# Kernel tuning notes

Hardware: AMD Instinct MI355X
Metric: run time of the kernel (lower is better)

## Reference

```python
import jax, jax.numpy as jnp
import numpy as np

N_NODES = 100000
N_EDGES = 1600000
NODE_DIM = 64
HIDDEN = 64
T = 11


def _init_linear(key, d_in, d_out, bias=True):
    kw, kb = jax.random.split(key)
    lim = 1.0 / np.sqrt(d_in)
    W = jax.random.uniform(kw, (d_in, d_out), jnp.float32, -lim, lim)
    if bias:
        b = jax.random.uniform(kb, (d_out,), jnp.float32, -lim, lim)
        return W, b
    return W


def setup_inputs() -> dict:
    key = jax.random.key(0)
    ks = jax.random.split(key, 10)
    x = jax.random.normal(ks[0], (N_NODES, NODE_DIM), jnp.float32)
    edge_index = jax.random.randint(ks[1], (2, N_EDGES), 0, N_NODES, jnp.int64)
    time_span = jnp.arange(T, dtype=jnp.float32)
    # SAGEConv params: W_neigh (lin_l, with bias) applied to mean-aggregated
    # neighbors, W_root (lin_r, no bias) applied to the node itself.
    W1n, b1 = _init_linear(ks[2], NODE_DIM, HIDDEN)
    W1r = _init_linear(ks[3], NODE_DIM, HIDDEN, bias=False)
    W2n, b2 = _init_linear(ks[4], HIDDEN, HIDDEN)
    W2r = _init_linear(ks[5], HIDDEN, HIDDEN, bias=False)
    W3n, b3 = _init_linear(ks[6], HIDDEN, NODE_DIM)
    W3r = _init_linear(ks[7], HIDDEN, NODE_DIM, bias=False)
    Wd, bd = _init_linear(ks[8], NODE_DIM, 2)
    return {
        "x": x, "edge_index": edge_index, "time_span": time_span,
        "W1n": W1n, "b1": b1, "W1r": W1r,
        "W2n": W2n, "b2": b2, "W2r": W2r,
        "W3n": W3n, "b3": b3, "W3r": W3r,
        "Wd": Wd, "bd": bd,
    }


def _sage_conv(x, src, dst, deg_inv, Wn, bn, Wr):
    # gather source features, mean-aggregate onto targets (PyG SAGEConv 'mean')
    agg = jax.ops.segment_sum(x[src], dst, num_segments=N_NODES)  # [N, d]
    mean = agg * deg_inv  # zero for isolated nodes
    return mean @ Wn + bn + x @ Wr


def reference(x, edge_index, time_span, W1n, b1, W1r, W2n, b2, W2r,
              W3n, b3, W3r, Wd, bd):
    src, dst = edge_index[0], edge_index[1]
    deg = jax.ops.segment_sum(jnp.ones((N_EDGES,), jnp.float32), dst,
                              num_segments=N_NODES)
    deg_inv = jnp.where(deg > 0, 1.0 / jnp.maximum(deg, 1.0), 0.0)[:, None]

    def ode_func(h):
        h1 = jax.nn.relu(_sage_conv(h, src, dst, deg_inv, W1n, b1, W1r))
        h2 = jax.nn.relu(_sage_conv(h1, src, dst, deg_inv, W2n, b2, W2r))
        return _sage_conv(h2, src, dst, deg_inv, W3n, b3, W3r)

    dts = time_span[1:] - time_span[:-1]  # euler fixed-step per interval

    def step(h, dt):
        h_new = h + dt * ode_func(h)
        return h_new, h_new

    _, xs = jax.lax.scan(step, x, dts)
    solution = jnp.concatenate([x[None], xs], axis=0)  # [T, N, node_dim]
    trajectories = solution @ Wd + bd  # [T, N, 2]
    return trajectories, solution
```

## Files before the change

### kernel.cpp

```cpp
#include <hip/hip_runtime.h>

#define NN 100000
#define NE 1600000
#define DIM 64
#define TT 11
#define NB_SCAN 391
#define NCH 13
#define CST 16

typedef unsigned short u16;
typedef unsigned int u32;

__device__ __forceinline__ u32 pack_bf16(float a, float b) {
    u32 ua = __float_as_uint(a);
    ua += 0x7fff + ((ua >> 16) & 1);
    u32 ub = __float_as_uint(b);
    ub += 0x7fff + ((ub >> 16) & 1);
    return (ua >> 16) | (ub & 0xffff0000u);
}
__device__ __forceinline__ float bf2f(u16 v) {
    return __uint_as_float(((u32)v) << 16);
}

__global__ void k_degc(const int* __restrict__ src, const int* __restrict__ dst,
                       int* __restrict__ deg, int* __restrict__ degc) {
    int e = blockIdx.x * blockDim.x + threadIdx.x;
    if (e < NE) {
        int d = dst[e], c = src[e] >> 13;
        atomicAdd(&deg[d], 1);
        atomicAdd(&degc[d * CST + c], 1);
    }
}

__global__ __launch_bounds__(256) void k_bsum(const int* __restrict__ deg,
                                              int* __restrict__ bsum) {
    __shared__ int s[256];
    int t = threadIdx.x;
    int i = blockIdx.x * 256 + t;
    s[t] = (i < NN) ? deg[i] : 0;
    __syncthreads();
    for (int off = 128; off >= 1; off >>= 1) {
        if (t < off) s[t] += s[t + off];
        __syncthreads();
    }
    if (t == 0) bsum[blockIdx.x] = s[0];
}

__global__ __launch_bounds__(512) void k_scan1(const int* __restrict__ bsum,
                                               int* __restrict__ bpre) {
    __shared__ int s[512];
    int t = threadIdx.x;
    int v0 = (t < NB_SCAN) ? bsum[t] : 0;
    s[t] = v0;
    __syncthreads();
    for (int off = 1; off < 512; off <<= 1) {
        int v = (t >= off) ? s[t - off] : 0;
        __syncthreads();
        s[t] += v;
        __syncthreads();
    }
    if (t < NB_SCAN) bpre[t] = s[t] - v0;
}

__global__ __launch_bounds__(256) void k_rowptr(const int* __restrict__ deg,
        const int* __restrict__ degc, const int* __restrict__ bpre,
        int* __restrict__ row_ptr, int* __restrict__ cursor16,
        float* __restrict__ deg_inv) {
    __shared__ int s[256];
    int t = threadIdx.x;
    int i = blockIdx.x * 256 + t;
    int d = (i < NN) ? deg[i] : 0;
    s[t] = d;
    __syncthreads();
    for (int off = 1; off < 256; off <<= 1) {
        int v = (t >= off) ? s[t - off] : 0;
        __syncthreads();
        s[t] += v;
        __syncthreads();
    }
    if (i < NN) {
        int excl = bpre[blockIdx.x] + s[t] - d;
        row_ptr[i] = excl;
        deg_inv[i] = d > 0 ? 1.0f / (float)d : 0.0f;
        int run = excl;
#pragma unroll
        for (int c = 0; c < NCH; ++c) {
            cursor16[i * CST + c] = run;
            run += degc[i * CST + c];
        }
        if (i == NN - 1) row_ptr[NN] = excl + d;
    }
}

__global__ void k_fillc(const int* __restrict__ src, const int* __restrict__ dst,
        int* __restrict__ cursor16, int* __restrict__ csr_src) {
    int e = blockIdx.x * blockDim.x + threadIdx.x;
    if (e < NE) {
        int sv = src[e];
        int p = atomicAdd(&cursor16[dst[e] * CST + (sv >> 13)], 1);
        csr_src[p] = sv;
    }
}

__global__ __launch_bounds__(256) void k_gather(const u16* __restrict__ hb,
        const int* __restrict__ row_ptr, const int* __restrict__ csr_src,
        const float* __restrict__ deg_inv, u16* __restrict__ Mb) {
    int wid = (int)((blockIdx.x * blockDim.x + threadIdx.x) >> 6);
    int lane = threadIdx.x & 63;
    if (wid >= NN) return;
    int sub = lane >> 3;
    int d4 = lane & 7;
    int b = row_ptr[wid], e = row_ptr[wid + 1];
    float di = deg_inv[wid];
    float a0[8] = {0, 0, 0, 0, 0, 0, 0, 0};
    float a1[8] = {0, 0, 0, 0, 0, 0, 0, 0};
    int i = b;
    for (; i + 16 <= e; i += 16) {
        int n0 = csr_src[i + sub];
        int n1 = csr_src[i + 8 + sub];
        uint4 v0 = *(const uint4*)(hb + ((size_t)n0 << 6) + d4 * 8);
        uint4 v1 = *(const uint4*)(hb + ((size_t)n1 << 6) + d4 * 8);
        const u32* w0 = (const u32*)&v0;
        const u32* w1 = (const u32*)&v1;
#pragma unroll
        for (int w = 0; w < 4; ++w) {
            a0[2 * w]     += __uint_as_float(w0[w] << 16);
            a0[2 * w + 1] += __uint_as_float(w0[w] & 0xffff0000u);
            a1[2 * w]     += __uint_as_float(w1[w] << 16);
            a1[2 * w + 1] += __uint_as_float(w1[w] & 0xffff0000u);
        }
    }
    if (i + 8 <= e) {
        int n0 = csr_src[i + sub];
        uint4 v0 = *(const uint4*)(hb + ((size_t)n0 << 6) + d4 * 8);
        const u32* w0 = (const u32*)&v0;
#pragma unroll
        for (int w = 0; w < 4; ++w) {
            a0[2 * w]     += __uint_as_float(w0[w] << 16);
            a0[2 * w + 1] += __uint_as_float(w0[w] & 0xffff0000u);
        }
        i += 8;
    }
    if (sub < e - i) {
        int n1 = csr_src[i + sub];
        uint4 v1 = *(const uint4*)(hb + ((size_t)n1 << 6) + d4 * 8);
        const u32* w1 = (const u32*)&v1;
#pragma unroll
        for (int w = 0; w < 4; ++w) {
            a1[2 * w]     += __uint_as_float(w1[w] << 16);
            a1[2 * w + 1] += __uint_as_float(w1[w] & 0xffff0000u);
        }
    }
    float s[8];
#pragma unroll
    for (int k = 0; k < 8; ++k) {
        float v = a0[k] + a1[k];
        v += __shfl_xor(v, 32);
        v += __shfl_xor(v, 16);
        v += __shfl_xor(v, 8);
        s[k] = v * di;
    }
    if (lane < 8) {
        uint4 p;
        p.x = pack_bf16(s[0], s[1]);
        p.y = pack_bf16(s[2], s[3]);
        p.z = pack_bf16(s[4], s[5]);
        p.w = pack_bf16(s[6], s[7]);
        *(uint4*)(Mb + ((size_t)wid << 6) + d4 * 8) = p;
    }
}

template <int MODE>
__global__ __launch_bounds__(256) void k_transform(
        const u16* __restrict__ Mb, const u16* __restrict__ Hb,
        const float* __restrict__ Wn, const float* __restrict__ bias,
        const float* __restrict__ Wr, const float* __restrict__ prev,
        const float* __restrict__ ts, int tstep, float* __restrict__ out,
        u16* __restrict__ out_b,
        const float* __restrict__ Wd, const float* __restrict__ bd,
        float* __restrict__ traj) {
    __shared__ float Ws[128 * 64];
    __shared__ float tp0[MODE ? 128 * 9 : 1];
    __shared__ float tp1[MODE ? 128 * 9 : 1];
    int tid = threadIdx.x;
    {
        const float4* wn4 = (const float4*)Wn;
        const float4* wr4 = (const float4*)Wr;
        float4* ws4 = (float4*)Ws;
        for (int i = tid; i < 2048; i += 256)
            ws4[i] = (i < 1024) ? wn4[i] : wr4[i - 1024];
    }
    __syncthreads();
    int jg = tid & 7, ng = tid >> 3;
    int nbase = blockIdx.x * 128 + ng * 4;
    int j0 = jg * 8;
    float acc[4][8];
#pragma unroll
    for (int i = 0; i < 4; ++i)
#pragma unroll
        for (int j = 0; j < 8; ++j) acc[i][j] = bias[j0 + j];
    int nidx[4];
    bool valid[4];
#pragma unroll
    for (int i = 0; i < 4; ++i) {
        int n = nbase + i;
        valid[i] = n < NN;
        nidx[i] = valid[i] ? n : 0;
    }
#pragma unroll 1
    for (int ph = 0; ph < 2; ++ph) {
        const u16* A = ph ? Hb : Mb;
        int wofs = ph ? 64 * 64 : 0;
        for (int k0 = 0; k0 < 64; k0 += 4) {
            float a[4][4];
#pragma unroll
            for (int i = 0; i < 4; ++i) {
                ushort4 r = *(const ushort4*)(A + ((size_t)nidx[i] << 6) + k0);
                a[i][0] = bf2f(r.x); a[i][1] = bf2f(r.y);
                a[i][2] = bf2f(r.z); a[i][3] = bf2f(r.w);
            }
#pragma unroll
            for (int kk = 0; kk < 4; ++kk) {
                float w[8];
                *(float4*)&w[0] = *(float4*)&Ws[wofs + (k0 + kk) * 64 + j0];
                *(float4*)&w[4] = *(float4*)&Ws[wofs + (k0 + kk) * 64 + j0 + 4];
#pragma unroll
                for (int i = 0; i < 4; ++i)
#pragma unroll
                    for (int j = 0; j < 8; ++j)
                        acc[i][j] = fmaf(a[i][kk], w[j], acc[i][j]);
            }
        }
    }
    float dt = 0.f, wd0[8], wd1[8];
    if (MODE == 1) {
        dt = ts[tstep + 1] - ts[tstep];
#pragma unroll
        for (int j = 0; j < 8; ++j) {
            wd0[j] = Wd[(j0 + j) * 2 + 0];
            wd1[j] = Wd[(j0 + j) * 2 + 1];
        }
    }
#pragma unroll
    for (int i = 0; i < 4; ++i) {
        float o[8];
        float p0 = 0.f, p1 = 0.f;
#pragma unroll
        for (int j = 0; j < 8; ++j) {
            float v = acc[i][j];
            if (MODE == 0) v = fmaxf(v, 0.f);
            else v = prev[(size_t)nidx[i] * 64 + j0 + j] + dt * v;
            o[j] = v;
            if (MODE == 1) { p0 = fmaf(v, wd0[j], p0); p1 = fmaf(v, wd1[j], p1); }
        }
        if (MODE == 1) {
            tp0[(ng * 4 + i) * 9 + jg] = p0;
            tp1[(ng * 4 + i) * 9 + jg] = p1;
        }
        if (valid[i]) {
            if (MODE == 1) {
                *(float4*)(out + (size_t)nidx[i] * 64 + j0) = *(float4*)&o[0];
                *(float4*)(out + (size_t)nidx[i] * 64 + j0 + 4) = *(float4*)&o[4];
            }
            uint4 pb;
            pb.x = pack_bf16(o[0], o[1]);
            pb.y = pack_bf16(o[2], o[3]);
            pb.z = pack_bf16(o[4], o[5]);
            pb.w = pack_bf16(o[6], o[7]);
            *(uint4*)(out_b + (size_t)nidx[i] * 64 + j0) = pb;
        }
    }
    if (MODE == 1) {
        __syncthreads();
        int node = tid >> 1, comp = tid & 1;
        const float* tp = comp ? tp1 : tp0;
        float s = bd[comp];
#pragma unroll
        for (int g = 0; g < 8; ++g) s += tp[node * 9 + g];
        int gnode = blockIdx.x * 128 + node;
        if (gnode < NN)
            traj[((size_t)(tstep + 1) * NN + gnode) * 2 + comp] = s;
    }
}

__global__ __launch_bounds__(256) void k_init(const float* __restrict__ x,
        const float* __restrict__ Wd, const float* __restrict__ bd,
        float* __restrict__ sol0, u16* __restrict__ xb,
        float* __restrict__ traj) {
    int n = blockIdx.x * blockDim.x + threadIdx.x;
    if (n >= NN) return;
    const float4* xr = (const float4*)(x + ((size_t)n << 6));
    float4* sr = (float4*)(sol0 + ((size_t)n << 6));
    uint4* br = (uint4*)(xb + ((size_t)n << 6));
    float p0 = bd[0], p1 = bd[1];
#pragma unroll
    for (int k8 = 0; k8 < 8; ++k8) {
        float4 v0 = xr[k8 * 2];
        float4 v1 = xr[k8 * 2 + 1];
        sr[k8 * 2] = v0;
        sr[k8 * 2 + 1] = v1;
        uint4 pb;
        pb.x = pack_bf16(v0.x, v0.y);
        pb.y = pack_bf16(v0.z, v0.w);
        pb.z = pack_bf16(v1.x, v1.y);
        pb.w = pack_bf16(v1.z, v1.w);
        br[k8] = pb;
        int k = k8 * 8;
        p0 = fmaf(v0.x, Wd[(k + 0) * 2], p0); p1 = fmaf(v0.x, Wd[(k + 0) * 2 + 1], p1);
        p0 = fmaf(v0.y, Wd[(k + 1) * 2], p0); p1 = fmaf(v0.y, Wd[(k + 1) * 2 + 1], p1);
        p0 = fmaf(v0.z, Wd[(k + 2) * 2], p0); p1 = fmaf(v0.z, Wd[(k + 2) * 2 + 1], p1);
        p0 = fmaf(v0.w, Wd[(k + 3) * 2], p0); p1 = fmaf(v0.w, Wd[(k + 3) * 2 + 1], p1);
        p0 = fmaf(v1.x, Wd[(k + 4) * 2], p0); p1 = fmaf(v1.x, Wd[(k + 4) * 2 + 1], p1);
        p0 = fmaf(v1.y, Wd[(k + 5) * 2], p0); p1 = fmaf(v1.y, Wd[(k + 5) * 2 + 1], p1);
        p0 = fmaf(v1.z, Wd[(k + 6) * 2], p0); p1 = fmaf(v1.z, Wd[(k + 6) * 2 + 1], p1);
        p0 = fmaf(v1.w, Wd[(k + 7) * 2], p0); p1 = fmaf(v1.w, Wd[(k + 7) * 2 + 1], p1);
    }
    traj[(size_t)n * 2 + 0] = p0;
    traj[(size_t)n * 2 + 1] = p1;
}

extern "C" void kernel_launch(void* const* d_in, const int* in_sizes, int n_in,
                              void* d_out, int out_size, void* d_ws, size_t ws_size,
                              hipStream_t stream) {
    const float* x = (const float*)d_in[0];
    const int* ei = (const int*)d_in[1];
    const float* ts = (const float*)d_in[2];
    const float* W1n = (const float*)d_in[3];
    const float* b1 = (const float*)d_in[4];
    const float* W1r = (const float*)d_in[5];
    const float* W2n = (const float*)d_in[6];
    const float* b2 = (const float*)d_in[7];
    const float* W2r = (const float*)d_in[8];
    const float* W3n = (const float*)d_in[9];
    const float* b3 = (const float*)d_in[10];
    const float* W3r = (const float*)d_in[11];
    const float* Wd = (const float*)d_in[12];
    const float* bd = (const float*)d_in[13];
    const int* src = ei;
    const int* dst = ei + NE;

    char* w = (char*)d_ws;
    int* deg = (int*)w;          w += (size_t)NN * 4;
    int* degc = (int*)w;         w += (size_t)NN * CST * 4;
    int* row_ptr = (int*)w;      w += (size_t)(NN + 1) * 4;
    int* cursor16 = (int*)w;     w += (size_t)NN * CST * 4;
    float* deg_inv = (float*)w;  w += (size_t)NN * 4;
    int* bsum = (int*)w;         w += (size_t)512 * 4;
    int* bpre = (int*)w;         w += (size_t)512 * 4;
    int* csr = (int*)w;          w += (size_t)NE * 4;
    u16* Mb = (u16*)w;           w += (size_t)NN * DIM * 2;
    u16* hb0 = (u16*)w;          w += (size_t)NN * DIM * 2;
    u16* hb1 = (u16*)w;          w += (size_t)NN * DIM * 2;
    u16* hb2 = (u16*)w;          w += (size_t)NN * DIM * 2;

    float* traj = (float*)d_out;
    float* sol = traj + (size_t)TT * NN * 2;

    hipMemsetAsync(deg, 0, (size_t)NN * (CST + 1) * 4, stream);
    k_degc<<<(NE + 255) / 256, 256, 0, stream>>>(src, dst, deg, degc);
    k_bsum<<<NB_SCAN, 256, 0, stream>>>(deg, bsum);
    k_scan1<<<1, 512, 0, stream>>>(bsum, bpre);
    k_rowptr<<<NB_SCAN, 256, 0, stream>>>(deg, degc, bpre, row_ptr, cursor16, deg_inv);
    k_fillc<<<(NE + 255) / 256, 256, 0, stream>>>(src, dst, cursor16, csr);
    k_init<<<NB_SCAN, 256, 0, stream>>>(x, Wd, bd, sol, hb0, traj);

    const int GB = (NN * 64 + 255) / 256;
    const int TB = (NN + 127) / 128;
    for (int t = 0; t < TT - 1; ++t) {
        float* st = sol + (size_t)t * NN * DIM;
        float* sn = st + (size_t)NN * DIM;
        k_gather<<<GB, 256, 0, stream>>>(hb0, row_ptr, csr, deg_inv, Mb);
        k_transform<0><<<TB, 256, 0, stream>>>(Mb, hb0, W1n, b1, W1r, nullptr,
                ts, t, nullptr, hb1, Wd, bd, traj);
        k_gather<<<GB, 256, 0, stream>>>(hb1, row_ptr, csr, deg_inv, Mb);
        k_transform<0><<<TB, 256, 0, stream>>>(Mb, hb1, W2n, b2, W2r, nullptr,
                ts, t, nullptr, hb2, Wd, bd, traj);
        k_gather<<<GB, 256, 0, stream>>>(hb2, row_ptr, csr, deg_inv, Mb);
        k_transform<1><<<TB, 256, 0, stream>>>(Mb, hb2, W3n, b3, W3r, st,
                ts, t, sn, hb0, Wd, bd, traj);
    }
}
```

Before: 2.725 ms.

## Gather 8 rows per wave with per-chunk neighbor counts for locality-ordered access

The gather kernel now assigns one 8-lane group per destination row, so a wave serves 8 rows instead of 1. Each group walks the row's neighbors chunk by chunk using stored per-source-chunk counts (u16 ccnt). Adjacent groups therefore touch source rows in the same 8192-node chunk at roughly the same time, which is meant to improve cache reuse and remove the cross-lane shuffle reduction. The separate degree array is dropped and degree is derived from degc. In exchange, lanes within a wave diverge when rows have different degrees or chunk counts, and each lane now issues one load at a time.

Measured after the change: 3.078 ms. 1.13x slower.

```diff
diff --git a/kernel.cpp b/kernel.cpp
--- a/kernel.cpp
+++ b/kernel.cpp
@@ -23,21 +23,22 @@
 }
 
 __global__ void k_degc(const int* __restrict__ src, const int* __restrict__ dst,
-                       int* __restrict__ deg, int* __restrict__ degc) {
+                       int* __restrict__ degc) {
     int e = blockIdx.x * blockDim.x + threadIdx.x;
-    if (e < NE) {
-        int d = dst[e], c = src[e] >> 13;
-        atomicAdd(&deg[d], 1);
-        atomicAdd(&degc[d * CST + c], 1);
-    }
-}
-
-__global__ __launch_bounds__(256) void k_bsum(const int* __restrict__ deg,
+    if (e < NE) atomicAdd(&degc[dst[e] * CST + (src[e] >> 13)], 1);
+}
+
+__global__ __launch_bounds__(256) void k_bsum(const int* __restrict__ degc,
                                               int* __restrict__ bsum) {
     __shared__ int s[256];
     int t = threadIdx.x;
     int i = blockIdx.x * 256 + t;
-    s[t] = (i < NN) ? deg[i] : 0;
+    int d = 0;
+    if (i < NN) {
+#pragma unroll
+        for (int c = 0; c < NCH; ++c) d += degc[i * CST + c];
+    }
+    s[t] = d;
     __syncthreads();
     for (int off = 128; off >= 1; off >>= 1) {
         if (t < off) s[t] += s[t + off];
@@ -62,14 +63,19 @@
     if (t < NB_SCAN) bpre[t] = s[t] - v0;
 }
 
-__global__ __launch_bounds__(256) void k_rowptr(const int* __restrict__ deg,
-        const int* __restrict__ degc, const int* __restrict__ bpre,
-        int* __restrict__ row_ptr, int* __restrict__ cursor16,
+__global__ __launch_bounds__(256) void k_rowptr(const int* __restrict__ degc,
+        const int* __restrict__ bpre, int* __restrict__ row_ptr,
+        int* __restrict__ cursor16, u16* __restrict__ ccnt,
         float* __restrict__ deg_inv) {
     __shared__ int s[256];
     int t = threadIdx.x;
     int i = blockIdx.x * 256 + t;
-    int d = (i < NN) ? deg[i] : 0;
+    int dc[NCH];
+    int d = 0;
+    if (i < NN) {
+#pragma unroll
+        for (int c = 0; c < NCH; ++c) { dc[c] = degc[i * CST + c]; d += dc[c]; }
+    }
     s[t] = d;
     __syncthreads();
     for (int off = 1; off < 256; off <<= 1) {
@@ -86,8 +92,11 @@
 #pragma unroll
         for (int c = 0; c < NCH; ++c) {
             cursor16[i * CST + c] = run;
-            run += degc[i * CST + c];
-        }
+            ccnt[i * CST + c] = (u16)dc[c];
+            run += dc[c];
+        }
+#pragma unroll
+        for (int c = NCH; c < CST; ++c) ccnt[i * CST + c] = 0;
         if (i == NN - 1) row_ptr[NN] = excl + d;
     }
 }
@@ -103,71 +112,43 @@
 }
 
 __global__ __launch_bounds__(256) void k_gather(const u16* __restrict__ hb,
-        const int* __restrict__ row_ptr, const int* __restrict__ csr_src,
-        const float* __restrict__ deg_inv, u16* __restrict__ Mb) {
-    int wid = (int)((blockIdx.x * blockDim.x + threadIdx.x) >> 6);
-    int lane = threadIdx.x & 63;
-    if (wid >= NN) return;
-    int sub = lane >> 3;
-    int d4 = lane & 7;
-    int b = row_ptr[wid], e = row_ptr[wid + 1];
-    float di = deg_inv[wid];
-    float a0[8] = {0, 0, 0, 0, 0, 0, 0, 0};
-    float a1[8] = {0, 0, 0, 0, 0, 0, 0, 0};
-    int i = b;
-    for (; i + 16 <= e; i += 16) {
-        int n0 = csr_src[i + sub];
-        int n1 = csr_src[i + 8 + sub];
-        uint4 v0 = *(const uint4*)(hb + ((size_t)n0 << 6) + d4 * 8);
-        uint4 v1 = *(const uint4*)(hb + ((size_t)n1 << 6) + d4 * 8);
-        const u32* w0 = (const u32*)&v0;
-        const u32* w1 = (const u32*)&v1;
-#pragma unroll
-        for (int w = 0; w < 4; ++w) {
-            a0[2 * w]     += __uint_as_float(w0[w] << 16);
-            a0[2 * w + 1] += __uint_as_float(w0[w] & 0xffff0000u);
-            a1[2 * w]     += __uint_as_float(w1[w] << 16);
-            a1[2 * w + 1] += __uint_as_float(w1[w] & 0xffff0000u);
-        }
-    }
-    if (i + 8 <= e) {
-        int n0 = csr_src[i + sub];
-        uint4 v0 = *(const uint4*)(hb + ((size_t)n0 << 6) + d4 * 8);
-        const u32* w0 = (const u32*)&v0;
-#pragma unroll
-        for (int w = 0; w < 4; ++w) {
-            a0[2 * w]     += __uint_as_float(w0[w] << 16);
-            a0[2 * w + 1] += __uint_as_float(w0[w] & 0xffff0000u);
-        }
-        i += 8;
-    }
-    if (sub < e - i) {
-        int n1 = csr_src[i + sub];
-        uint4 v1 = *(const uint4*)(hb + ((size_t)n1 << 6) + d4 * 8);
-        const u32* w1 = (const u32*)&v1;
-#pragma unroll
-        for (int w = 0; w < 4; ++w) {
-            a1[2 * w]     += __uint_as_float(w1[w] << 16);
-            a1[2 * w + 1] += __uint_as_float(w1[w] & 0xffff0000u);
-        }
-    }
-    float s[8];
-#pragma unroll
-    for (int k = 0; k < 8; ++k) {
-        float v = a0[k] + a1[k];
-        v += __shfl_xor(v, 32);
-        v += __shfl_xor(v, 16);
-        v += __shfl_xor(v, 8);
-        s[k] = v * di;
-    }
-    if (lane < 8) {
-        uint4 p;
-        p.x = pack_bf16(s[0], s[1]);
-        p.y = pack_bf16(s[2], s[3]);
-        p.z = pack_bf16(s[4], s[5]);
-        p.w = pack_bf16(s[6], s[7]);
-        *(uint4*)(Mb + ((size_t)wid << 6) + d4 * 8) = p;
-    }
+        const int* __restrict__ row_ptr, const u16* __restrict__ ccnt,
+        const int* __restrict__ csr_src, const float* __restrict__ deg_inv,
+        u16* __restrict__ Mb) {
+    int tid = threadIdx.x;
+    int wv = tid >> 6, lane = tid & 63;
+    int g = lane >> 3, d4 = lane & 7;
+    int row = blockIdx.x * 32 + wv * 8 + g;
+    int pos = row_ptr[row];
+    const uint4* cq = (const uint4*)(ccnt + row * CST);
+    uint4 q0 = cq[0];
+    uint4 q1 = cq[1];
+    u32 cw[8] = {q0.x, q0.y, q0.z, q0.w, q1.x, q1.y, q1.z, q1.w};
+    float acc[8] = {0, 0, 0, 0, 0, 0, 0, 0};
+#pragma unroll
+    for (int c = 0; c < NCH; ++c) {
+        int cnt = (int)((cw[c >> 1] >> ((c & 1) * 16)) & 0xffffu);
+        for (int k = 0; k < cnt; ++k) {
+            int nb = csr_src[pos + k];
+            uint4 v = *(const uint4*)(hb + ((size_t)nb << 6) + (d4 << 3));
+            acc[0] += __uint_as_float(v.x << 16);
+            acc[1] += __uint_as_float(v.x & 0xffff0000u);
+            acc[2] += __uint_as_float(v.y << 16);
+            acc[3] += __uint_as_float(v.y & 0xffff0000u);
+            acc[4] += __uint_as_float(v.z << 16);
+            acc[5] += __uint_as_float(v.z & 0xffff0000u);
+            acc[6] += __uint_as_float(v.w << 16);
+            acc[7] += __uint_as_float(v.w & 0xffff0000u);
+        }
+        pos += cnt;
+    }
+    float di = deg_inv[row];
+    uint4 p;
+    p.x = pack_bf16(acc[0] * di, acc[1] * di);
+    p.y = pack_bf16(acc[2] * di, acc[3] * di);
+    p.z = pack_bf16(acc[4] * di, acc[5] * di);
+    p.w = pack_bf16(acc[6] * di, acc[7] * di);
+    *(uint4*)(Mb + ((size_t)row << 6) + (d4 << 3)) = p;
 }
 
 template <int MODE>
@@ -340,10 +321,10 @@
     const int* dst = ei + NE;
 
     char* w = (char*)d_ws;
-    int* deg = (int*)w;          w += (size_t)NN * 4;
     int* degc = (int*)w;         w += (size_t)NN * CST * 4;
     int* row_ptr = (int*)w;      w += (size_t)(NN + 1) * 4;
     int* cursor16 = (int*)w;     w += (size_t)NN * CST * 4;
+    u16* ccnt = (u16*)w;         w += (size_t)NN * CST * 2;
     float* deg_inv = (float*)w;  w += (size_t)NN * 4;
     int* bsum = (int*)w;         w += (size_t)512 * 4;
     int* bpre = (int*)w;         w += (size_t)512 * 4;
@@ -356,26 +337,26 @@
     float* traj = (float*)d_out;
     float* sol = traj + (size_t)TT * NN * 2;
 
-    hipMemsetAsync(deg, 0, (size_t)NN * (CST + 1) * 4, stream);
-    k_degc<<<(NE + 255) / 256, 256, 0, stream>>>(src, dst, deg, degc);
-    k_bsum<<<NB_SCAN, 256, 0, stream>>>(deg, bsum);
+    hipMemsetAsync(degc, 0, (size_t)NN * CST * 4, stream);
+    k_degc<<<(NE + 255) / 256, 256, 0, stream>>>(src, dst, degc);
+    k_bsum<<<NB_SCAN, 256, 0, stream>>>(degc, bsum);
     k_scan1<<<1, 512, 0, stream>>>(bsum, bpre);
-    k_rowptr<<<NB_SCAN, 256, 0, stream>>>(deg, degc, bpre, row_ptr, cursor16, deg_inv);
+    k_rowptr<<<NB_SCAN, 256, 0, stream>>>(degc, bpre, row_ptr, cursor16, ccnt, deg_inv);
     k_fillc<<<(NE + 255) / 256, 256, 0, stream>>>(src, dst, cursor16, csr);
     k_init<<<NB_SCAN, 256, 0, stream>>>(x, Wd, bd, sol, hb0, traj);
 
-    const int GB = (NN * 64 + 255) / 256;
+    const int GB = NN / 32;
     const int TB = (NN + 127) / 128;
     for (int t = 0; t < TT - 1; ++t) {
         float* st = sol + (size_t)t * NN * DIM;
         float* sn = st + (size_t)NN * DIM;
-        k_gather<<<GB, 256, 0, stream>>>(hb0, row_ptr, csr, deg_inv, Mb);
+        k_gather<<<GB, 256, 0, stream>>>(hb0, row_ptr, ccnt, csr, deg_inv, Mb);
         k_transform<0><<<TB, 256, 0, stream>>>(Mb, hb0, W1n, b1, W1r, nullptr,
                 ts, t, nullptr, hb1, Wd, bd, traj);
-        k_gather<<<GB, 256, 0, stream>>>(hb1, row_ptr, csr, deg_inv, Mb);
+        k_gather<<<GB, 256, 0, stream>>>(hb1, row_ptr, ccnt, csr, deg_inv, Mb);
         k_transform<0><<<TB, 256, 0, stream>>>(Mb, hb1, W2n, b2, W2r, nullptr,
                 ts, t, nullptr, hb2, Wd, bd, traj);
-        k_gather<<<GB, 256, 0, stream>>>(hb2, row_ptr, csr, deg_inv, Mb);
+        k_gather<<<GB, 256, 0, stream>>>(hb2, row_ptr, ccnt, csr, deg_inv, Mb);
         k_transform<1><<<TB, 256, 0, stream>>>(Mb, hb2, W3n, b3, W3r, st,
                 ts, t, sn, hb0, Wd, bd, traj);
     }
```
